# Kernel tuning notes

Hardware: AMD Instinct MI355X
Metric: run time of the kernel (lower is better)

## Reference

```python
import jax, jax.numpy as jnp
import numpy as np

HEADS = 8
DH_QK = 32
DH_V = 32
BS = 8          # block_size
HALO = 3
WIN = BS + 2 * HALO  # 14
REL = 2 * WIN - 1    # 27
SCALE = DH_QK ** -0.5


def setup_inputs() -> dict:
    key = jax.random.key(0)
    k1, k2, k3, k4, k5 = jax.random.split(key, 5)
    dim = 256
    dim_out_qk = HEADS * DH_QK  # 256
    dim_out_v = HEADS * DH_V    # 256
    std = dim ** -0.5
    x = jax.random.normal(k1, (4, dim, 128, 128), jnp.float32)
    w_q = jax.random.normal(k2, (dim_out_qk, dim), jnp.float32) * std
    w_kv = jax.random.normal(k3, (dim_out_qk + dim_out_v, dim), jnp.float32) * std
    height_rel = jax.random.normal(k4, (REL, DH_QK), jnp.float32) * SCALE
    width_rel = jax.random.normal(k5, (REL, DH_QK), jnp.float32) * SCALE
    return {"x": x, "w_q": w_q, "w_kv": w_kv, "height_rel": height_rel, "width_rel": width_rel}


def rel_logits_1d(q, rel_k, permute):
    N, H, W, d = q.shape
    rel_size = rel_k.shape[0]
    win = (rel_size + 1) // 2
    x = jnp.einsum('nhwd,rd->nhwr', q, rel_k)
    x = x.reshape(-1, W, rel_size)
    x = jnp.pad(x, ((0, 0), (0, 0), (0, 1))).reshape(x.shape[0], -1)
    x = jnp.pad(x, ((0, 0), (0, rel_size - W)))
    x = x.reshape(-1, W + 1, rel_size)
    x = x[:, :W, win - 1:]
    x = x.reshape(N, H, 1, W, win)
    x = jnp.broadcast_to(x, (N, H, win, W, win))
    return x.transpose(permute)


def pos_embed_rel(q, height_rel, width_rel):
    # q: (BH, nblocks, bs*bs, dh)
    B, BB, HW, dh = q.shape
    qb = q.reshape(-1, BS, BS, dh)
    rel_w = rel_logits_1d(qb, width_rel, (0, 1, 3, 2, 4))
    rel_h = rel_logits_1d(qb.transpose(0, 2, 1, 3), height_rel, (0, 3, 1, 4, 2))
    return (rel_h + rel_w).reshape(B, BB, HW, -1)


def reference(x, w_q, w_kv, height_rel, width_rel):
    B, C, H, W = x.shape
    nh, nw = H // BS, W // BS
    nb = nh * nw
    # 1x1 conv projections as einsum
    q = jnp.einsum('bchw,oc->bohw', x, w_q)
    # (B*heads, nb, bs*bs, dh_qk), queries row-major within block, blocks row-major
    q = q.reshape(B * HEADS, DH_QK, nh, BS, nw, BS).transpose(0, 2, 4, 3, 5, 1)
    q = q.reshape(B * HEADS, nb, BS * BS, DH_QK)
    kv = jnp.einsum('bchw,oc->bohw', x, w_kv)
    kv = jnp.pad(kv, ((0, 0), (0, 0), (HALO, HALO), (HALO, HALO)))
    # halo windows via gather (unfold)
    ih = np.arange(nh)[:, None] * BS + np.arange(WIN)[None, :]
    iw = np.arange(nw)[:, None] * BS + np.arange(WIN)[None, :]
    kv = kv[:, :, ih]
    kv = kv[:, :, :, :, iw]
    kv = kv.transpose(0, 1, 2, 4, 3, 5)
    kv = kv.reshape(B * HEADS, DH_QK + DH_V, nb, WIN * WIN).transpose(0, 2, 3, 1)
    k = kv[..., :DH_QK]
    v = kv[..., DH_QK:]
    attn = jnp.einsum('bnqd,bnkd->bnqk', q, k) * SCALE + pos_embed_rel(q, height_rel, width_rel)
    attn = jax.nn.softmax(attn, axis=-1)
    out = jnp.einsum('bnqk,bnkd->bnqd', attn, v)
    # (BH, nb, HW, dv) -> (B, heads*dv, H, W)
    out = out.transpose(0, 3, 2, 1)  # (BH, dv, HW, nb)
    out = out.reshape(-1, BS, BS, nh, nw).transpose(0, 3, 1, 4, 2)
    out = out.reshape(B, HEADS * DH_V, H, W)
    return out
```

## Files before the change

kernel.cpp:

```cpp
#include <hip/hip_runtime.h>
#include <stdint.h>

#define HEADS 8
#define DH    32
#define BSZ   8
#define HALO  3
#define WIN   14
#define NKEY  196
#define CIN   256
#define IMG   128
#define HWPIX 16384
#define MQKV  768
#define SCALE 0.17677669529663689f

#define KS_STRIDE 36
#define VT_STRIDE 212
#define PQ_STRIDE 120
#define QB_STRIDE 68

typedef short bf16x8 __attribute__((ext_vector_type(8)));
typedef short bf16x4 __attribute__((ext_vector_type(4)));
typedef float f32x4  __attribute__((ext_vector_type(4)));

#define AS1 __attribute__((address_space(1)))
#define AS3 __attribute__((address_space(3)))

__device__ __forceinline__ void gl_lds16(const void* g, void* l) {
  __builtin_amdgcn_global_load_lds((AS1 const unsigned int*)g,
                                   (AS3 unsigned int*)l, 16, 0, 0);
}

__device__ __forceinline__ float bf2f(unsigned short s){ return __uint_as_float(((unsigned int)s) << 16); }
__device__ __forceinline__ unsigned short f2bf(float f){
  unsigned int u = __float_as_uint(f);
  u += 0x7fffu + ((u >> 16) & 1u);
  return (unsigned short)(u >> 16);
}

__device__ __forceinline__ bf16x8 ld2(const unsigned short* p) {
  bf16x4 a = *(const bf16x4*)p;
  bf16x4 b = *(const bf16x4*)(p + 4);
  bf16x8 r;
  r[0]=a[0]; r[1]=a[1]; r[2]=a[2]; r[3]=a[3];
  r[4]=b[0]; r[5]=b[1]; r[6]=b[2]; r[7]=b[3];
  return r;
}

__device__ __forceinline__ void st_bf4(unsigned short* p, f32x4 c) {
  ushort4 o;
  o.x = f2bf(c[0]); o.y = f2bf(c[1]); o.z = f2bf(c[2]); o.w = f2bf(c[3]);
  *(ushort4*)p = o;
}

__global__ void convw_kernel(const float* __restrict__ wq,
                             const float* __restrict__ wkv,
                             unsigned short* __restrict__ Wb)
{
  int idx = blockIdx.x * 256 + threadIdx.x;
  int m = idx >> 6, c4 = idx & 63;
  int h = m / 96, d = m - h * 96;
  const float* src = (d < 32) ? wq  + (size_t)(h * 32 + d) * CIN
                              : wkv + (size_t)(h * 64 + d - 32) * CIN;
  float4 v = *(const float4*)(src + c4 * 4);
  ushort4 o;
  o.x = f2bf(v.x); o.y = f2bf(v.y); o.z = f2bf(v.z); o.w = f2bf(v.w);
  *(ushort4*)(Wb + (size_t)m * CIN + c4 * 4) = o;
}

__global__ void convrel_kernel(const float* __restrict__ hrel,
                               const float* __restrict__ wrel,
                               unsigned short* __restrict__ relb)
{
  int idx = blockIdx.x * 256 + threadIdx.x;
  int r = idx >> 5, c = idx & 31;
  float v = 0.f;
  if (r < 27) v = hrel[r * 32 + c];
  else if (r >= 32 && r < 59) v = wrel[(r - 32) * 32 + c];
  relb[idx] = f2bf(v);
}

__global__ __launch_bounds__(256)
void convx_kernel(const float* __restrict__ x, unsigned short* __restrict__ xb)
{
  __shared__ unsigned short T[64 * 264];
  const int tid = threadIdx.x;
  const int p0 = blockIdx.x * 64;
  const float* xin = x + (size_t)blockIdx.y * CIN * HWPIX;
  unsigned short* xo = xb + ((size_t)blockIdx.y * HWPIX + p0) * CIN;

  for (int idx = tid; idx < 2048; idx += 256) {
    int cp = idx >> 4, f = idx & 15;
    const float* r0 = xin + (size_t)(2 * cp) * HWPIX + p0 + f * 4;
    float4 a = *(const float4*)r0;
    float4 b = *(const float4*)(r0 + HWPIX);
    unsigned short* tp = T + (4 * f) * 264 + 2 * cp;
    *(unsigned int*)(tp      ) = (unsigned int)f2bf(a.x) | ((unsigned int)f2bf(b.x) << 16);
    *(unsigned int*)(tp + 264) = (unsigned int)f2bf(a.y) | ((unsigned int)f2bf(b.y) << 16);
    *(unsigned int*)(tp + 528) = (unsigned int)f2bf(a.z) | ((unsigned int)f2bf(b.z) << 16);
    *(unsigned int*)(tp + 792) = (unsigned int)f2bf(a.w) | ((unsigned int)f2bf(b.w) << 16);
  }
  __syncthreads();
  for (int idx = tid; idx < 2048; idx += 256) {
    int p = idx >> 5, u = idx & 31;
    *(uint4*)(xo + (size_t)p * CIN + u * 8) = *(const uint4*)(T + p * 264 + u * 8);
  }
}

__global__ __launch_bounds__(256, 3)
void proj_kernel(const unsigned short* __restrict__ xb,
                 const unsigned short* __restrict__ Wb,
                 unsigned short* __restrict__ qkv)
{
  __shared__ unsigned short As[128 * 64];
  __shared__ unsigned short Bs[128 * 64];

  const int tid = threadIdx.x;
  const int w = tid >> 6, lane = tid & 63;
  const int g16 = lane >> 4, l15 = lane & 15;
  const int m0 = blockIdx.x * 128;
  const int bl = blockIdx.y >> 7;
  const int p0 = (blockIdx.y & 127) * 128;
  const int wm = w >> 1, wn = w & 1;
  const unsigned short* xrow = xb + ((size_t)bl * HWPIX + p0) * CIN;

  f32x4 acc[4][4];
  #pragma unroll
  for (int i = 0; i < 4; ++i)
    #pragma unroll
    for (int j = 0; j < 4; ++j) acc[i][j] = (f32x4){0.f,0.f,0.f,0.f};

  for (int kk = 0; kk < 4; ++kk) {
    const int k0 = kk * 64;
    #pragma unroll
    for (int c = 0; c < 4; ++c) {
      int ci = w * 4 + c;
      gl_lds16(Wb   + (size_t)(m0 + ci*8 + (lane>>3)) * CIN + k0 + (lane&7)*8, As + ci*512);
      gl_lds16(xrow + (size_t)(     ci*8 + (lane>>3)) * CIN + k0 + (lane&7)*8, Bs + ci*512);
    }
    __syncthreads();

    #pragma unroll
    for (int kh = 0; kh < 2; ++kh) {
      bf16x8 af[4], bfr[4];
      #pragma unroll
      for (int t = 0; t < 4; ++t) {
        af[t]  = *(const bf16x8*)(As + (wm*64 + t*16 + l15)*64 + kh*32 + g16*8);
        bfr[t] = *(const bf16x8*)(Bs + (wn*64 + t*16 + l15)*64 + kh*32 + g16*8);
      }
      #pragma unroll
      for (int tm = 0; tm < 4; ++tm)
        #pragma unroll
        for (int tn = 0; tn < 4; ++tn)
          acc[tm][tn] = __builtin_amdgcn_mfma_f32_16x16x32_bf16(
                          af[tm], bfr[tn], acc[tm][tn], 0, 0, 0);
    }
    __syncthreads();
  }

  #pragma unroll
  for (int tm = 0; tm < 4; ++tm) {
    int ch = m0 + wm*64 + tm*16 + g16*4;
    #pragma unroll
    for (int tn = 0; tn < 4; ++tn) {
      int pix = p0 + wn*64 + tn*16 + l15;
      st_bf4(qkv + ((size_t)bl * HWPIX + pix) * MQKV + ch, acc[tm][tn]);
    }
  }
}

__global__ __launch_bounds__(256, 3)
void attn_kernel(const unsigned short* __restrict__ qkv,
                 const unsigned short* __restrict__ relb,
                 float* __restrict__ out,
                 int b0)
{
  __shared__ unsigned short Ks[208 * KS_STRIDE];
  __shared__ unsigned short Vt[32 * VT_STRIDE];
  __shared__ unsigned short Pq[64 * PQ_STRIDE];
  __shared__ unsigned short QB[64 * QB_STRIDE];

  const int tid = threadIdx.x;
  const int by = blockIdx.x >> 4, bx = blockIdx.x & 15;
  const int hd = blockIdx.y, bb = blockIdx.z;
  const size_t pixbase = (size_t)bb * HWPIX;

  const int w = tid >> 6, lane = tid & 63;
  const int g16 = lane >> 4, l15 = lane & 15;
  const int q = w * 16 + l15;
  const int qy = q >> 3, qx = q & 7;
  const int gy = by * BSZ + qy, gx = bx * BSZ + qx;

  bf16x8 qf = *(const bf16x8*)(qkv + (pixbase + (size_t)gy * IMG + gx) * MQKV + hd * 96 + g16 * 8);

  *(uint4*)(Pq + tid * 8) = *(const uint4*)(relb + tid * 8);

  for (int i = tid; i < 432; i += 256) Ks[196 * KS_STRIDE + i] = 0;
  for (int i = tid; i < 512; i += 256) Vt[(i >> 4) * VT_STRIDE + 196 + (i & 15)] = 0;

  for (int idx = tid; idx < NKEY * 8; idx += 256) {
    int key = idx >> 3, part = idx & 7;
    int ky = key / WIN, kx = key - ky * WIN;
    int sy = by * BSZ - HALO + ky, sx = bx * BSZ - HALO + kx;
    uint4 val = make_uint4(0,0,0,0);
    if ((unsigned)sy < (unsigned)IMG && (unsigned)sx < (unsigned)IMG)
      val = *(const uint4*)(qkv + (pixbase + sy * IMG + sx) * MQKV + hd * 96 + 32 + part * 8);
    if (part < 4) {
      unsigned short* kp = Ks + key * KS_STRIDE + part * 8;
      *(unsigned long long*)(kp    ) = (unsigned long long)val.x | ((unsigned long long)val.y << 32);
      *(unsigned long long*)(kp + 4) = (unsigned long long)val.z | ((unsigned long long)val.w << 32);
    } else {
      int dh0 = (part - 4) * 8;
      unsigned int u[4] = {val.x, val.y, val.z, val.w};
      #pragma unroll
      for (int e = 0; e < 4; ++e) {
        Vt[(dh0 + 2*e    ) * VT_STRIDE + key] = (unsigned short)(u[e] & 0xffffu);
        Vt[(dh0 + 2*e + 1) * VT_STRIDE + key] = (unsigned short)(u[e] >> 16);
      }
    }
  }
  __syncthreads();

  {
    const unsigned short* Hb = Pq;
    const unsigned short* Wr = Pq + 1024;
    bf16x8 ah0 = *(const bf16x8*)(Hb + l15 * 32 + g16 * 8);
    bf16x8 ah1 = *(const bf16x8*)(Hb + (16 + l15) * 32 + g16 * 8);
    bf16x8 aw0 = *(const bf16x8*)(Wr + l15 * 32 + g16 * 8);
    bf16x8 aw1 = *(const bf16x8*)(Wr + (16 + l15) * 32 + g16 * 8);
    f32x4 z = (f32x4){0.f,0.f,0.f,0.f};
    f32x4 ch0 = __builtin_amdgcn_mfma_f32_16x16x32_bf16(ah0, qf, z, 0, 0, 0);
    f32x4 ch1 = __builtin_amdgcn_mfma_f32_16x16x32_bf16(ah1, qf, z, 0, 0, 0);
    f32x4 cw0 = __builtin_amdgcn_mfma_f32_16x16x32_bf16(aw0, qf, z, 0, 0, 0);
    f32x4 cw1 = __builtin_amdgcn_mfma_f32_16x16x32_bf16(aw1, qf, z, 0, 0, 0);
    unsigned short* QBq = QB + q * QB_STRIDE;
    st_bf4(QBq      + g16 * 4, ch0);
    st_bf4(QBq + 16 + g16 * 4, ch1);
    st_bf4(QBq + 32 + g16 * 4, cw0);
    st_bf4(QBq + 48 + g16 * 4, cw1);
  }
  __syncthreads();

  const unsigned short* QBq = QB + q * QB_STRIDE;
  unsigned short* Prow = Pq + q * PQ_STRIDE;

  float lsum = 0.f;
  f32x4 o0 = (f32x4){0.f,0.f,0.f,0.f}, o1 = (f32x4){0.f,0.f,0.f,0.f};
  const f32x4 z = (f32x4){0.f,0.f,0.f,0.f};

  #pragma unroll
  for (int half = 0; half < 2; ++half) {
    const int t0 = half ? 7 : 0;
    const int ntiles = half ? 6 : 7;
    #pragma unroll
    for (int u = 0; u < ntiles; ++u) {
      int nt = t0 + u;
      bf16x8 kf = ld2(Ks + (nt * 16 + l15) * KS_STRIDE + g16 * 8);
      f32x4 c = __builtin_amdgcn_mfma_f32_16x16x32_bf16(kf, qf, z, 0, 0, 0);
      float pv[4];
      #pragma unroll
      for (int i = 0; i < 4; ++i) {
        int key = nt * 16 + g16 * 4 + i;
        int ky = key / WIN, kx = key - ky * WIN;
        float s = c[i] * SCALE + bf2f(QBq[ky - qy + 13]) + bf2f(QBq[32 + kx - qx + 13]);
        float p = (key < NKEY) ? __expf(s) : 0.f;
        lsum += p;
        pv[i] = p;
      }
      ushort4 pk;
      pk.x = f2bf(pv[0]); pk.y = f2bf(pv[1]); pk.z = f2bf(pv[2]); pk.w = f2bf(pv[3]);
      *(ushort4*)(Prow + u * 16 + g16 * 4) = pk;
    }
    const int nch = half ? 3 : 4;
    #pragma unroll
    for (int cc = 0; cc < nch; ++cc) {
      bf16x8 pf = (bf16x8){0,0,0,0,0,0,0,0};
      bool masked = (half == 0 && cc == 3);
      if (!masked || g16 < 2)
        pf = *(const bf16x8*)(Prow + cc * 32 + g16 * 8);
      int vcol = (half ? 112 : 0) + cc * 32 + g16 * 8;
      bf16x8 v0 = ld2(Vt + l15 * VT_STRIDE + vcol);
      bf16x8 v1 = ld2(Vt + (16 + l15) * VT_STRIDE + vcol);
      o0 = __builtin_amdgcn_mfma_f32_16x16x32_bf16(v0, pf, o0, 0, 0, 0);
      o1 = __builtin_amdgcn_mfma_f32_16x16x32_bf16(v1, pf, o1, 0, 0, 0);
    }
  }

  lsum += __shfl_xor(lsum, 16);
  lsum += __shfl_xor(lsum, 32);
  float inv = 1.f / lsum;

  float* ob = out + (((size_t)(b0 + bb) * 256 + hd * DH) * HWPIX) + (size_t)gy * IMG + gx;
  #pragma unroll
  for (int i = 0; i < 4; ++i) {
    int dh0 = g16 * 4 + i;
    ob[(size_t)dh0 * HWPIX]        = o0[i] * inv;
    ob[(size_t)(dh0 + 16) * HWPIX] = o1[i] * inv;
  }
}

extern "C" void kernel_launch(void* const* d_in, const int* in_sizes, int n_in,
                              void* d_out, int out_size, void* d_ws, size_t ws_size,
                              hipStream_t stream)
{
  (void)in_sizes; (void)n_in; (void)out_size;
  const float* x    = (const float*)d_in[0];
  const float* wq   = (const float*)d_in[1];
  const float* wkv  = (const float*)d_in[2];
  const float* hrel = (const float*)d_in[3];
  const float* wrel = (const float*)d_in[4];
  float* out = (float*)d_out;

  const size_t wb_bytes   = (size_t)MQKV * CIN * 2;
  const size_t relb_bytes = 4096;
  const size_t xb_per_b   = (size_t)HWPIX * CIN * 2;
  const size_t qkv_per_b  = (size_t)HWPIX * MQKV * 2;
  const int chunk = (ws_size >= wb_bytes + relb_bytes + 4 * (xb_per_b + qkv_per_b)) ? 4 : 1;

  unsigned short* Wb   = (unsigned short*)d_ws;
  unsigned short* relb = (unsigned short*)((char*)d_ws + wb_bytes);
  unsigned short* xb   = (unsigned short*)((char*)d_ws + wb_bytes + relb_bytes);
  unsigned short* qkv  = (unsigned short*)((char*)d_ws + wb_bytes + relb_bytes
                                           + (size_t)chunk * xb_per_b);

  convw_kernel<<<192, 256, 0, stream>>>(wq, wkv, Wb);
  convrel_kernel<<<8, 256, 0, stream>>>(hrel, wrel, relb);

  for (int b0 = 0; b0 < 4; b0 += chunk) {
    convx_kernel<<<dim3(256, chunk), 256, 0, stream>>>(x + (size_t)b0 * CIN * HWPIX, xb);
    proj_kernel<<<dim3(6, 128 * chunk), 256, 0, stream>>>(xb, Wb, qkv);
    attn_kernel<<<dim3(256, HEADS, chunk), 256, 0, stream>>>(qkv, relb, out, b0);
  }
}
```

Before: 274.9 us.

## Pad key window to 14x16 grid and use exp2 softmax with packed bf16 conversion

Changes the key layout in shared memory from 196 contiguous keys to a 14x16 padded grid, so each 16-key tile is one window row. Row and column indices become shifts instead of divides, the height bias is loaded once per tile, and padded columns are masked with a precomputed -inf width bias instead of per-element compares. The softmax uses exp2 with a fused scale and hardware packed bf16 conversion. In exchange it does more MFMA tiles (14 instead of 13), adds extra global-load iterations for the padding slots, and grows shared memory use.

```diff
diff --git a/kernel.cpp b/kernel.cpp
--- a/kernel.cpp
+++ b/kernel.cpp
@@ -14,9 +14,9 @@
 #define SCALE 0.17677669529663689f
 
 #define KS_STRIDE 36
-#define VT_STRIDE 212
+#define VT_STRIDE 228
 #define PQ_STRIDE 120
-#define QB_STRIDE 68
+#define QB_STRIDE 64
 
 typedef short bf16x8 __attribute__((ext_vector_type(8)));
 typedef short bf16x4 __attribute__((ext_vector_type(4)));
@@ -174,7 +174,7 @@
                  float* __restrict__ out,
                  int b0)
 {
-  __shared__ unsigned short Ks[208 * KS_STRIDE];
+  __shared__ unsigned short Ks[224 * KS_STRIDE];
   __shared__ unsigned short Vt[32 * VT_STRIDE];
   __shared__ unsigned short Pq[64 * PQ_STRIDE];
   __shared__ unsigned short QB[64 * QB_STRIDE];
@@ -194,15 +194,12 @@
 
   *(uint4*)(Pq + tid * 8) = *(const uint4*)(relb + tid * 8);
 
-  for (int i = tid; i < 432; i += 256) Ks[196 * KS_STRIDE + i] = 0;
-  for (int i = tid; i < 512; i += 256) Vt[(i >> 4) * VT_STRIDE + 196 + (i & 15)] = 0;
-
-  for (int idx = tid; idx < NKEY * 8; idx += 256) {
+  for (int idx = tid; idx < 224 * 8; idx += 256) {
     int key = idx >> 3, part = idx & 7;
-    int ky = key / WIN, kx = key - ky * WIN;
+    int ky = key >> 4, kx = key & 15;
     int sy = by * BSZ - HALO + ky, sx = bx * BSZ - HALO + kx;
     uint4 val = make_uint4(0,0,0,0);
-    if ((unsigned)sy < (unsigned)IMG && (unsigned)sx < (unsigned)IMG)
+    if (kx < WIN && (unsigned)sy < (unsigned)IMG && (unsigned)sx < (unsigned)IMG)
       val = *(const uint4*)(qkv + (pixbase + sy * IMG + sx) * MQKV + hd * 96 + 32 + part * 8);
     if (part < 4) {
       unsigned short* kp = Ks + key * KS_STRIDE + part * 8;
@@ -243,41 +240,46 @@
   const unsigned short* QBq = QB + q * QB_STRIDE;
   unsigned short* Prow = Pq + q * PQ_STRIDE;
 
+  const float LOG2E = 1.4426950408889634f;
+  const float SL2E  = SCALE * LOG2E;
+
+  float bw2[4];
+  #pragma unroll
+  for (int i = 0; i < 4; ++i) {
+    int kx = g16 * 4 + i;
+    bw2[i] = (kx < WIN) ? bf2f(QBq[32 + kx - qx + 13]) * LOG2E : -1e30f;
+  }
+
   float lsum = 0.f;
   f32x4 o0 = (f32x4){0.f,0.f,0.f,0.f}, o1 = (f32x4){0.f,0.f,0.f,0.f};
   const f32x4 z = (f32x4){0.f,0.f,0.f,0.f};
 
   #pragma unroll
   for (int half = 0; half < 2; ++half) {
-    const int t0 = half ? 7 : 0;
-    const int ntiles = half ? 6 : 7;
-    #pragma unroll
-    for (int u = 0; u < ntiles; ++u) {
-      int nt = t0 + u;
+    #pragma unroll
+    for (int u = 0; u < 7; ++u) {
+      const int nt = half * 7 + u;
       bf16x8 kf = ld2(Ks + (nt * 16 + l15) * KS_STRIDE + g16 * 8);
       f32x4 c = __builtin_amdgcn_mfma_f32_16x16x32_bf16(kf, qf, z, 0, 0, 0);
-      float pv[4];
-      #pragma unroll
-      for (int i = 0; i < 4; ++i) {
-        int key = nt * 16 + g16 * 4 + i;
-        int ky = key / WIN, kx = key - ky * WIN;
-        float s = c[i] * SCALE + bf2f(QBq[ky - qy + 13]) + bf2f(QBq[32 + kx - qx + 13]);
-        float p = (key < NKEY) ? __expf(s) : 0.f;
-        lsum += p;
-        pv[i] = p;
-      }
-      ushort4 pk;
-      pk.x = f2bf(pv[0]); pk.y = f2bf(pv[1]); pk.z = f2bf(pv[2]); pk.w = f2bf(pv[3]);
-      *(ushort4*)(Prow + u * 16 + g16 * 4) = pk;
-    }
-    const int nch = half ? 3 : 4;
-    #pragma unroll
-    for (int cc = 0; cc < nch; ++cc) {
+      float bh2 = bf2f(QBq[nt - qy + 13]) * LOG2E;
+      float p0 = exp2f(fmaf(c[0], SL2E, bh2 + bw2[0]));
+      float p1 = exp2f(fmaf(c[1], SL2E, bh2 + bw2[1]));
+      float p2 = exp2f(fmaf(c[2], SL2E, bh2 + bw2[2]));
+      float p3 = exp2f(fmaf(c[3], SL2E, bh2 + bw2[3]));
+      lsum += (p0 + p1) + (p2 + p3);
+      unsigned int plo, phi;
+      asm("v_cvt_pk_bf16_f32 %0, %1, %2" : "=v"(plo) : "v"(p0), "v"(p1));
+      asm("v_cvt_pk_bf16_f32 %0, %1, %2" : "=v"(phi) : "v"(p2), "v"(p3));
+      *(uint2*)(Prow + u * 16 + g16 * 4) = make_uint2(plo, phi);
+    }
+    #pragma unroll
+    for (int cc = 0; cc < 4; ++cc) {
       bf16x8 pf = (bf16x8){0,0,0,0,0,0,0,0};
-      bool masked = (half == 0 && cc == 3);
+      const bool masked = (cc == 3);
       if (!masked || g16 < 2)
         pf = *(const bf16x8*)(Prow + cc * 32 + g16 * 8);
-      int vcol = (half ? 112 : 0) + cc * 32 + g16 * 8;
+      int vcol = half * 112 + cc * 32 + g16 * 8;
+      if (masked && g16 >= 2) vcol = 0;
       bf16x8 v0 = ld2(Vt + l15 * VT_STRIDE + vcol);
       bf16x8 v1 = ld2(Vt + (16 + l15) * VT_STRIDE + vcol);
       o0 = __builtin_amdgcn_mfma_f32_16x16x32_bf16(v0, pf, o0, 0, 0, 0);
```

Result: slower. 306.4 us (+11.5%).
